# Optimization experiments

Hardware: AMD Instinct MI355X
Metric: run time of the kernel (lower is better)

The kernel has to match this reference:

```python
import jax, jax.numpy as jnp
import numpy as np
import math

B, H, N, D = 8, 8, 4096, 64
M = 64          # select_number (CUR rank)
N_ITER = 6      # Newton-Schulz iterations in iterative_inv


def setup_inputs() -> dict:
    key = jax.random.key(0)
    k1, k2, k3 = jax.random.split(key, 3)
    Q = jax.random.normal(k1, (B, H, N, D), jnp.float32)
    K = jax.random.normal(k2, (B, H, N, D), jnp.float32)
    V = jax.random.normal(k3, (B, H, N, D), jnp.float32)
    mask = jnp.ones((B, N), dtype=bool)
    return {"Q": Q, "K": K, "V": V, "mask": mask}


def _top_k_sum_select(T, mask, m):
    # select_type='sum', absolute=False -> score = row sum over D
    somme = T.sum(-1)                                    # [B,H,N]
    somme = jnp.where(mask[:, None, :], somme, -jnp.finfo(somme.dtype).max)
    idx = jnp.argsort(-somme, axis=-1)[..., :m]          # descending top-m, [B,H,M]
    nt = jnp.take_along_axis(T, idx[..., None], axis=2)  # [B,H,M,D]
    return nt, idx


def _iterative_inv(mat, n_iter=N_ITER):
    # init_option='original': global-max scaled transpose
    m = mat.shape[-1]
    I = jnp.eye(m, dtype=mat.dtype)
    Km = mat
    Vm = Km.swapaxes(-1, -2) / jnp.max(Km.sum(-2))
    for _ in range(n_iter):
        KV = Km @ Vm
        Vm = 0.25 * Vm @ (13.0 * I - KV @ (15.0 * I - KV @ (7.0 * I - KV)))
    return Vm


def reference(Q, K, V, mask):
    Qs = Q / math.sqrt(D)
    nc, _ = _top_k_sum_select(K, mask, M)        # column landmarks of K
    nr, r_idx = _top_k_sum_select(Qs, mask, M)   # row landmarks of Q
    c = jnp.einsum('bhnd,bhmd->bhnm', Qs, nc)    # [B,H,N,M]
    r = jnp.einsum('bhmd,bhnd->bhmn', nr, K)     # [B,H,M,N]
    r = jnp.where(mask[:, None, None, :], r, -jnp.finfo(r.dtype).max)
    kernel_1 = jax.nn.softmax(c, axis=-1)        # [B,H,N,M]
    # m_matrix_composition: gather rows of kernel_1 at r_idx -> [B,H,M,M]
    u = jnp.take_along_axis(kernel_1, r_idx[..., None], axis=2)
    kernel_3 = jax.nn.softmax(r, axis=-1)        # [B,H,M,N]
    kernel_2_inv = _iterative_inv(u)             # [B,H,M,M]
    RV = kernel_3 @ V                            # [B,H,M,D]
    X = kernel_1 @ (kernel_2_inv @ RV)           # [B,H,N,D]
    return X
```

## Files before the change

kernel.cpp:

```cpp
#include <hip/hip_runtime.h>
#include <math.h>

#define NSEQ 4096

#define OFF_SUMK 0u
#define OFF_SUMQ 262144u
#define OFF_WTH  0u
#define OFF_WTL  131072u
#define OFF_U    262144u
#define OFF_NC   524288u
#define OFF_NR   786432u
#define OFF_VM   1048576u
#define OFF_NCH  1310720u
#define OFF_NCL  1441792u
#define OFF_PMAX 1572864u
#define OFF_PSUM 1638400u
#define OFF_HMAX 1703936u
#define OFF_PRV  1704000u

typedef unsigned short u16;
typedef short short8 __attribute__((ext_vector_type(8)));
typedef short bf4 __attribute__((ext_vector_type(4)));
typedef float f32x4 __attribute__((ext_vector_type(4)));

__device__ __forceinline__ u16 f2bf(float x) {
    unsigned u = __float_as_uint(x);
    unsigned r = (u + 0x7FFFu + ((u >> 16) & 1u)) >> 16;
    return (u16)r;
}
__device__ __forceinline__ void splitbf(float x, u16& h, u16& l) {
    unsigned u = __float_as_uint(x);
    h = (u16)(u >> 16);
    float hf = __uint_as_float(u & 0xFFFF0000u);
    l = f2bf(x - hf);
}

__device__ __forceinline__ short8 ldfrag(const u16* base, int row, int k0) {
    int byte = (row << 7) + (k0 << 1);
    byte ^= (row & 7) << 4;
    return *(const short8*)((const char*)base + byte);
}
__device__ __forceinline__ void st4(u16* base, int row, int c0, ushort4 v) {
    int byte = (row << 7) + (c0 << 1);
    byte ^= (row & 7) << 4;
    *(ushort4*)((char*)base + byte) = v;
}
__device__ __forceinline__ void stb16(u16* base, int row, int c, u16 v) {
    int byte = (row << 7) + (c << 1);
    byte ^= (row & 7) << 4;
    *(u16*)((char*)base + byte) = v;
}
__device__ __forceinline__ unsigned vt_byte(int d, int n) {
    unsigned byte = ((unsigned)d << 7) + ((unsigned)n << 1);
    byte ^= ((d & 7) << 4) | ((d & 8) << 3);
    return byte;
}

__device__ __forceinline__ f32x4 MFMA(short8 a, short8 b, f32x4 c) {
    return __builtin_amdgcn_mfma_f32_16x16x32_bf16(a, b, c, 0, 0, 0);
}

__device__ __forceinline__ void stage64(const float* __restrict__ g, u16* Lh, u16* Ll,
                                        int t, float scale) {
#pragma unroll
    for (int i = 0; i < 4; i++) {
        int e = t + 256 * i;
        int row = e >> 4, c0 = (e & 15) << 2;
        float4 v = *(const float4*)(g + row * 64 + c0);
        float vv[4] = {v.x * scale, v.y * scale, v.z * scale, v.w * scale};
        ushort4 h, l;
        splitbf(vv[0], h.x, l.x); splitbf(vv[1], h.y, l.y);
        splitbf(vv[2], h.z, l.z); splitbf(vv[3], h.w, l.w);
        st4(Lh, row, c0, h); st4(Ll, row, c0, l);
    }
}

__device__ __forceinline__ void copy64bf(u16* dst, const u16* __restrict__ src, int t) {
#pragma unroll
    for (int i = 0; i < 4; i++) {
        int e = t + 256 * i;
        int row = e >> 4, c0 = (e & 15) << 2;
        ushort4 v = *(const ushort4*)(src + row * 64 + c0);
        st4(dst, row, c0, v);
    }
}

__device__ __forceinline__ void loadT64(float* dst, const float* __restrict__ src, int t) {
    for (int e = t; e < 1024; e += 256) {
        int m = e >> 4, k0 = (e & 15) << 2;
        float4 v = *(const float4*)(src + m * 64 + k0);
        dst[(k0 + 0) * 64 + m] = v.x;
        dst[(k0 + 1) * 64 + m] = v.y;
        dst[(k0 + 2) * 64 + m] = v.z;
        dst[(k0 + 3) * 64 + m] = v.w;
    }
}
__device__ __forceinline__ void mm64add(const float* Acm, const float* Brm,
                                        float acc[4][4], int i0, int j0) {
#pragma unroll 8
    for (int k = 0; k < 64; k++) {
        float4 a = *(const float4*)(Acm + k * 64 + i0);
        float4 b = *(const float4*)(Brm + k * 64 + j0);
        acc[0][0] += a.x * b.x; acc[0][1] += a.x * b.y; acc[0][2] += a.x * b.z; acc[0][3] += a.x * b.w;
        acc[1][0] += a.y * b.x; acc[1][1] += a.y * b.y; acc[1][2] += a.y * b.z; acc[1][3] += a.y * b.w;
        acc[2][0] += a.z * b.x; acc[2][1] += a.z * b.y; acc[2][2] += a.z * b.z; acc[2][3] += a.z * b.w;
        acc[3][0] += a.w * b.x; acc[3][1] += a.w * b.y; acc[3][2] += a.w * b.z; acc[3][3] += a.w * b.w;
    }
}
__device__ __forceinline__ void mm64(const float* Acm, const float* Brm,
                                     float acc[4][4], int i0, int j0) {
#pragma unroll
    for (int r = 0; r < 4; r++)
#pragma unroll
        for (int c = 0; c < 4; c++) acc[r][c] = 0.f;
    mm64add(Acm, Brm, acc, i0, j0);
}
__device__ __forceinline__ void writeN64(float* dst, const float acc[4][4], int i0, int j0, float s) {
#pragma unroll
    for (int r = 0; r < 4; r++) {
        float4 v;
        v.x = s * acc[r][0]; v.y = s * acc[r][1]; v.z = s * acc[r][2]; v.w = s * acc[r][3];
        *(float4*)(dst + (i0 + r) * 64 + j0) = v;
    }
}

__global__ __launch_bounds__(256) void k_sums(const float* __restrict__ Qg,
                                              const float* __restrict__ Kg, float* ws) {
    size_t row = (size_t)blockIdx.x * 64 + (threadIdx.x >> 2);
    int q = threadIdx.x & 3;
    const float4* qp = (const float4*)(Qg + row * 64 + q * 16);
    const float4* kp = (const float4*)(Kg + row * 64 + q * 16);
    float s1 = 0.f, s2 = 0.f;
#pragma unroll
    for (int i = 0; i < 4; i++) { float4 v = qp[i]; s1 += (v.x + v.y) + (v.z + v.w); }
#pragma unroll
    for (int i = 0; i < 4; i++) { float4 v = kp[i]; s2 += (v.x + v.y) + (v.z + v.w); }
    s1 += __shfl_xor(s1, 1); s1 += __shfl_xor(s1, 2);
    s2 += __shfl_xor(s2, 1); s2 += __shfl_xor(s2, 2);
    if (q == 0) { ws[OFF_SUMQ + row] = s1; ws[OFF_SUMK + row] = s2; }
}

__global__ __launch_bounds__(256) void k_select(const float* __restrict__ Qg,
                                                const float* __restrict__ Kg, float* ws) {
    int head = blockIdx.x, sel = blockIdx.y, t = threadIdx.x;
    __shared__ int hist[257];
    __shared__ int idx_s[64];
    __shared__ unsigned s_prefix;
    __shared__ int s_need, s_cnt, s_win;
    __shared__ int wred[4];
    const float* scores = ws + (sel ? OFF_SUMQ : OFF_SUMK) + (size_t)head * 4096;
    unsigned uu[16];
#pragma unroll
    for (int i = 0; i < 16; i++) {
        unsigned u = __float_as_uint(scores[t + 256 * i]);
        uu[i] = (u & 0x80000000u) ? ~u : (u | 0x80000000u);
    }
    if (t == 0) { s_prefix = 0u; s_need = 64; }
    __syncthreads();
#pragma unroll
    for (int p = 0; p < 4; p++) {
        hist[t] = 0;
        if (t == 0) hist[256] = 0;
        __syncthreads();
        unsigned pref = s_prefix;
        int sh = 32 - 8 * p;
        int dsh = 24 - 8 * p;
#pragma unroll
        for (int i = 0; i < 16; i++) {
            bool active = (p == 0) || ((uu[i] >> sh) == (pref >> sh));
            if (active) atomicAdd(&hist[(uu[i] >> dsh) & 255], 1);
        }
        __syncthreads();
        for (int s = 1; s < 256; s <<= 1) {
            int v = (t + s < 256) ? hist[t + s] : 0;
            __syncthreads();
            hist[t] += v;
            __syncthreads();
        }
        int need = s_need;
        __syncthreads();
        if (hist[t] >= need && (t == 255 || hist[t + 1] < need)) {
            s_need = need - ((t == 255) ? 0 : hist[t + 1]);
            s_prefix = pref | ((unsigned)t << dsh);
        }
        __syncthreads();
    }
    unsigned thr = s_prefix;
    int needEq = s_need;
    if (t == 0) s_cnt = 0;
    __syncthreads();
    unsigned eqm = 0;
#pragma unroll
    for (int i = 0; i < 16; i++) {
        if (uu[i] > thr) { int pos = atomicAdd(&s_cnt, 1); idx_s[pos] = t + 256 * i; }
        else if (uu[i] == thr) eqm |= (1u << i);
    }
    __syncthreads();
    int base = 64 - needEq;
    int lane = t & 63, wid = t >> 6;
    for (int r = 0; r < needEq; r++) {
        int mymin = 0x7FFFFFFF;
#pragma unroll
        for (int i = 0; i < 16; i++)
            if ((eqm >> i) & 1) mymin = min(mymin, t + 256 * i);
#pragma unroll
        for (int s = 1; s < 64; s <<= 1) mymin = min(mymin, __shfl_xor(mymin, s));
        if (lane == 0) wred[wid] = mymin;
        __syncthreads();
        if (t == 0) {
            int wv = min(min(wred[0], wred[1]), min(wred[2], wred[3]));
            s_win = wv;
            idx_s[base + r] = wv;
        }
        __syncthreads();
        int wv = s_win;
        if ((wv & 255) == t) eqm &= ~(1u << (wv >> 8));
        __syncthreads();
    }
    const float* src = sel ? Qg : Kg;
    float* dst = ws + (sel ? OFF_NR : OFF_NC) + (size_t)head * 4096;
    u16* dh = (u16*)(ws + OFF_NCH) + (size_t)head * 4096;
    u16* dl = (u16*)(ws + OFF_NCL) + (size_t)head * 4096;
    float scl = sel ? 0.125f : 1.0f;
    for (int e = t; e < 4096; e += 256) {
        int m = e >> 6, d = e & 63;
        float v = src[((size_t)head * NSEQ + (size_t)idx_s[m]) * 64 + d] * scl;
        dst[e] = v;
        if (!sel) { u16 h, l; splitbf(v, h, l); dh[e] = h; dl[e] = l; }
    }
}

__global__ __launch_bounds__(256) void k_u(float* ws) {
    int head = blockIdx.x, t = threadIdx.x;
    __shared__ __align__(16) float A_s[4096];
    __shared__ __align__(16) float B_s[4096];
    __shared__ float colpart[1024];
    loadT64(A_s, ws + OFF_NR + (size_t)head * 4096, t);
    loadT64(B_s, ws + OFF_NC + (size_t)head * 4096, t);
    __syncthreads();
    int ti = t >> 4, tj = t & 15, i0 = ti << 2, j0 = tj << 2;
    float acc[4][4];
    mm64(A_s, B_s, acc, i0, j0);
#pragma unroll
    for (int r = 0; r < 4; r++) {
        float m0 = fmaxf(fmaxf(acc[r][0], acc[r][1]), fmaxf(acc[r][2], acc[r][3]));
        m0 = fmaxf(m0, __shfl_xor(m0, 1)); m0 = fmaxf(m0, __shfl_xor(m0, 2));
        m0 = fmaxf(m0, __shfl_xor(m0, 4)); m0 = fmaxf(m0, __shfl_xor(m0, 8));
        float s = 0.f;
#pragma unroll
        for (int c = 0; c < 4; c++) { acc[r][c] = __expf(acc[r][c] - m0); s += acc[r][c]; }
        s += __shfl_xor(s, 1); s += __shfl_xor(s, 2);
        s += __shfl_xor(s, 4); s += __shfl_xor(s, 8);
#pragma unroll
        for (int c = 0; c < 4; c++) acc[r][c] = acc[r][c] / s;
    }
    float* u = ws + OFF_U + (size_t)head * 4096;
#pragma unroll
    for (int r = 0; r < 4; r++) {
        float4 v; v.x = acc[r][0]; v.y = acc[r][1]; v.z = acc[r][2]; v.w = acc[r][3];
        *(float4*)(u + (i0 + r) * 64 + j0) = v;
    }
#pragma unroll
    for (int c = 0; c < 4; c++)
        colpart[ti * 64 + j0 + c] = acc[0][c] + acc[1][c] + acc[2][c] + acc[3][c];
    __syncthreads();
    if (t < 64) {
        float cs = 0.f;
#pragma unroll
        for (int g = 0; g < 16; g++) cs += colpart[g * 64 + t];
        float v = cs;
#pragma unroll
        for (int s = 1; s < 64; s <<= 1) v = fmaxf(v, __shfl_xor(v, s));
        if (t == 0) ws[OFF_HMAX + head] = v;
    }
}

__global__ __launch_bounds__(256) void k_nsinv(float* ws) {
    int head = blockIdx.x, t = threadIdx.x;
    __shared__ __align__(16) u16 KmH[4096], KmL[4096];
    __shared__ __align__(16) u16 VmNH[4096], VmNL[4096];
    __shared__ __align__(16) u16 VmTH[4096], VmTL[4096];
    __shared__ __align__(16) u16 KVH[4096], KVL[4096];
    __shared__ __align__(16) u16 BtH[4096], BtL[4096];
    __shared__ __align__(16) float Vmf[4096];

    int w = t >> 6, lane = t & 63, lrow = lane & 15, lk = (lane >> 4) << 3;
    int mrow0 = 16 * w + ((lane >> 4) << 2);

    float g = ws[OFF_HMAX + lane];
#pragma unroll
    for (int s = 1; s < 64; s <<= 1) g = fmaxf(g, __shfl_xor(g, s));
    float ginv = 1.0f / g;

    const float* u = ws + OFF_U + (size_t)head * 4096;
#pragma unroll
    for (int i = 0; i < 4; i++) {
        int e = t + 256 * i;
        int row = e >> 4, c0 = (e & 15) << 2;
        float4 v = *(const float4*)(u + row * 64 + c0);
        float vv[4] = {v.x, v.y, v.z, v.w};
        ushort4 h4, l4;
        splitbf(vv[0], h4.x, l4.x); splitbf(vv[1], h4.y, l4.y);
        splitbf(vv[2], h4.z, l4.z); splitbf(vv[3], h4.w, l4.w);
        st4(KmH, row, c0, h4); st4(KmL, row, c0, l4);
        float sv[4] = {vv[0] * ginv, vv[1] * ginv, vv[2] * ginv, vv[3] * ginv};
        splitbf(sv[0], h4.x, l4.x); splitbf(sv[1], h4.y, l4.y);
        splitbf(sv[2], h4.z, l4.z); splitbf(sv[3], h4.w, l4.w);
        st4(VmTH, row, c0, h4); st4(VmTL, row, c0, l4);
#pragma unroll
        for (int k = 0; k < 4; k++) {
            u16 h, l; splitbf(sv[k], h, l);
            stb16(VmNH, c0 + k, row, h); stb16(VmNL, c0 + k, row, l);
            Vmf[(c0 + k) * 64 + row] = sv[k];
        }
    }
    __syncthreads();

    f32x4 cv[4];
    for (int it = 0; it < 6; it++) {
        {
            short8 a0h = ldfrag(KmH, 16 * w + lrow, lk);
            short8 a0l = ldfrag(KmL, 16 * w + lrow, lk);
            short8 a1h = ldfrag(KmH, 16 * w + lrow, 32 + lk);
            short8 a1l = ldfrag(KmL, 16 * w + lrow, 32 + lk);
#pragma unroll
            for (int nt = 0; nt < 4; nt++) {
                f32x4 acc = (f32x4){0.f, 0.f, 0.f, 0.f};
                short8 bh = ldfrag(VmTH, 16 * nt + lrow, lk);
                short8 bl = ldfrag(VmTL, 16 * nt + lrow, lk);
                acc = MFMA(a0h, bh, acc); acc = MFMA(a0l, bh, acc); acc = MFMA(a0h, bl, acc);
                bh = ldfrag(VmTH, 16 * nt + lrow, 32 + lk);
                bl = ldfrag(VmTL, 16 * nt + lrow, 32 + lk);
                acc = MFMA(a1h, bh, acc); acc = MFMA(a1l, bh, acc); acc = MFMA(a1h, bl, acc);
                cv[nt] = acc;
            }
        }
#pragma unroll
        for (int nt = 0; nt < 4; nt++)
#pragma unroll
            for (int j = 0; j < 4; j++) {
                int m = mrow0 + j, n = 16 * nt + lrow;
                float v = cv[nt][j];
                u16 h, l; splitbf(v, h, l);
                stb16(KVH, m, n, h); stb16(KVL, m, n, l);
                float b = ((m == n) ? 7.f : 0.f) - v;
                splitbf(b, h, l);
                stb16(BtH, n, m, h); stb16(BtL, n, m, l);
            }
        __syncthreads();
        {
            short8 a0h = ldfrag(KVH, 16 * w + lrow, lk);
            short8 a0l = ldfrag(KVL, 16 * w + lrow, lk);
            short8 a1h = ldfrag(KVH, 16 * w + lrow, 32 + lk);
            short8 a1l = ldfrag(KVL, 16 * w + lrow, 32 + lk);
#pragma unroll
            for (int nt = 0; nt < 4; nt++) {
                f32x4 acc = (f32x4){0.f, 0.f, 0.f, 0.f};
                short8 bh = ldfrag(BtH, 16 * nt + lrow, lk);
                short8 bl = ldfrag(BtL, 16 * nt + lrow, lk);
                acc = MFMA(a0h, bh, acc); acc = MFMA(a0l, bh, acc); acc = MFMA(a0h, bl, acc);
                bh = ldfrag(BtH, 16 * nt + lrow, 32 + lk);
                bl = ldfrag(BtL, 16 * nt + lrow, 32 + lk);
                acc = MFMA(a1h, bh, acc); acc = MFMA(a1l, bh, acc); acc = MFMA(a1h, bl, acc);
                cv[nt] = acc;
            }
        }
        __syncthreads();
#pragma unroll
        for (int nt = 0; nt < 4; nt++)
#pragma unroll
            for (int j = 0; j < 4; j++) {
                int m = mrow0 + j, n = 16 * nt + lrow;
                float b = ((m == n) ? 15.f : 0.f) - cv[nt][j];
                u16 h, l; splitbf(b, h, l);
                stb16(BtH, n, m, h); stb16(BtL, n, m, l);
            }
        __syncthreads();
        {
            short8 a0h = ldfrag(KVH, 16 * w + lrow, lk);
            short8 a0l = ldfrag(KVL, 16 * w + lrow, lk);
            short8 a1h = ldfrag(KVH, 16 * w + lrow, 32 + lk);
            short8 a1l = ldfrag(KVL, 16 * w + lrow, 32 + lk);
#pragma unroll
            for (int nt = 0; nt < 4; nt++) {
                f32x4 acc = (f32x4){0.f, 0.f, 0.f, 0.f};
                short8 bh = ldfrag(BtH, 16 * nt + lrow, lk);
                short8 bl = ldfrag(BtL, 16 * nt + lrow, lk);
                acc = MFMA(a0h, bh, acc); acc = MFMA(a0l, bh, acc); acc = MFMA(a0h, bl, acc);
                bh = ldfrag(BtH, 16 * nt + lrow, 32 + lk);
                bl = ldfrag(BtL, 16 * nt + lrow, 32 + lk);
                acc = MFMA(a1h, bh, acc); acc = MFMA(a1l, bh, acc); acc = MFMA(a1h, bl, acc);
                cv[nt] = acc;
            }
        }
        __syncthreads();
#pragma unroll
        for (int nt = 0; nt < 4; nt++)
#pragma unroll
            for (int j = 0; j < 4; j++) {
                int m = mrow0 + j, n = 16 * nt + lrow;
                float b = ((m == n) ? 13.f : 0.f) - cv[nt][j];
                u16 h, l; splitbf(b, h, l);
                stb16(BtH, n, m, h); stb16(BtL, n, m, l);
            }
        __syncthreads();
        {
            short8 a0h = ldfrag(VmNH, 16 * w + lrow, lk);
            short8 a0l = ldfrag(VmNL, 16 * w + lrow, lk);
            short8 a1h = ldfrag(VmNH, 16 * w + lrow, 32 + lk);
            short8 a1l = ldfrag(VmNL, 16 * w + lrow, 32 + lk);
#pragma unroll
            for (int nt = 0; nt < 4; nt++) {
                f32x4 acc = (f32x4){0.f, 0.f, 0.f, 0.f};
                short8 bh = ldfrag(BtH, 16 * nt + lrow, lk);
                short8 bl = ldfrag(BtL, 16 * nt + lrow, lk);
                acc = MFMA(a0h, bh, acc); acc = MFMA(a0l, bh, acc); acc = MFMA(a0h, bl, acc);
                bh = ldfrag(BtH, 16 * nt + lrow, 32 + lk);
                bl = ldfrag(BtL, 16 * nt + lrow, 32 + lk);
                acc = MFMA(a1h, bh, acc); acc = MFMA(a1l, bh, acc); acc = MFMA(a1h, bl, acc);
                cv[nt] = acc;
            }
        }
        __syncthreads();
#pragma unroll
        for (int nt = 0; nt < 4; nt++)
#pragma unroll
            for (int j = 0; j < 4; j++) {
                int m = mrow0 + j, n = 16 * nt + lrow;
                float v = 0.25f * cv[nt][j];
                u16 h, l; splitbf(v, h, l);
                stb16(VmNH, m, n, h); stb16(VmNL, m, n, l);
                stb16(VmTH, n, m, h); stb16(VmTL, n, m, l);
                Vmf[m * 64 + n] = v;
            }
        __syncthreads();
    }

    float* vm = ws + OFF_VM + (size_t)head * 4096;
#pragma unroll
    for (int i = 0; i < 4; i++) {
        int e = t + 256 * i;
        int row = e >> 4, c0 = (e & 15) << 2;
        *(float4*)(vm + row * 64 + c0) = *(const float4*)(Vmf + row * 64 + c0);
    }
}

__global__ __launch_bounds__(256) void k_rvp(const float* __restrict__ Kg,
                                             const float* __restrict__ Vg, float* ws) {
    int head = blockIdx.x, ch = blockIdx.y, t = threadIdx.x;
    int nch = gridDim.y;
    int nsub = (NSEQ / 64) / nch;
    __shared__ __align__(16) u16 Kh[4096], Kl[4096];
    __shared__ __align__(16) u16 Vth[4096], Vtl[4096];
    int w = t >> 6, lane = t & 63, lrow = lane & 15, g = lane >> 4;
    int lk = g << 3;
    int mrow0 = 16 * w + (g << 2);

    short8 nh0, nl0, nh1, nl1;
    {
        const float* nr = ws + OFF_NR + (size_t)head * 4096 + (size_t)(16 * w + lrow) * 64;
        float a[8], b[8];
        *(float4*)(a + 0) = *(const float4*)(nr + lk);
        *(float4*)(a + 4) = *(const float4*)(nr + lk + 4);
        *(float4*)(b + 0) = *(const float4*)(nr + 32 + lk);
        *(float4*)(b + 4) = *(const float4*)(nr + 32 + lk + 4);
#pragma unroll
        for (int i = 0; i < 8; i++) {
            u16 h, l;
            splitbf(a[i], h, l); nh0[i] = (short)h; nl0[i] = (short)l;
            splitbf(b[i], h, l); nh1[i] = (short)h; nl1[i] = (short)l;
        }
    }

    f32x4 rv[4];
#pragma unroll
    for (int dt = 0; dt < 4; dt++) rv[dt] = (f32x4){0.f, 0.f, 0.f, 0.f};
    float mrow = -INFINITY, srow = 0.f;

    int rows = NSEQ / nch;
    const float* Kb = Kg + ((size_t)head * NSEQ + (size_t)ch * rows) * 64;
    const float* Vb = Vg + ((size_t)head * NSEQ + (size_t)ch * rows) * 64;
    int vd = lane;
    int nb4 = (t >> 6) << 2;

    for (int s8 = 0; s8 < nsub; s8++) {
        __syncthreads();
        stage64(Kb + s8 * 4096, Kh, Kl, t, 1.0f);
        const float* Vs = Vb + s8 * 4096;
#pragma unroll
        for (int i = 0; i < 4; i++) {
            int n0 = nb4 + 16 * i;
            float x0 = Vs[(n0 + 0) * 64 + vd];
            float x1 = Vs[(n0 + 1) * 64 + vd];
            float x2 = Vs[(n0 + 2) * 64 + vd];
            float x3 = Vs[(n0 + 3) * 64 + vd];
            ushort4 h4, l4;
            splitbf(x0, h4.x, l4.x); splitbf(x1, h4.y, l4.y);
            splitbf(x2, h4.z, l4.z); splitbf(x3, h4.w, l4.w);
            *(ushort4*)((char*)Vth + vt_byte(vd, n0)) = h4;
            *(ushort4*)((char*)Vtl + vt_byte(vd, n0)) = l4;
        }
        __syncthreads();

        f32x4 cv[4];
#pragma unroll
        for (int nt = 0; nt < 4; nt++) {
            f32x4 acc = (f32x4){0.f, 0.f, 0.f, 0.f};
            short8 ah = ldfrag(Kh, 16 * nt + lrow, lk);
            short8 al = ldfrag(Kl, 16 * nt + lrow, lk);
            acc = MFMA(ah, nh0, acc); acc = MFMA(al, nh0, acc); acc = MFMA(ah, nl0, acc);
            ah = ldfrag(Kh, 16 * nt + lrow, 32 + lk);
            al = ldfrag(Kl, 16 * nt + lrow, 32 + lk);
            acc = MFMA(ah, nh1, acc); acc = MFMA(al, nh1, acc); acc = MFMA(ah, nl1, acc);
            cv[nt] = acc;
        }
        float m0 = cv[0][0];
#pragma unroll
        for (int nt = 0; nt < 4; nt++)
#pragma unroll
            for (int j = 0; j < 4; j++) m0 = fmaxf(m0, cv[nt][j]);
        m0 = fmaxf(m0, __shfl_xor(m0, 16));
        m0 = fmaxf(m0, __shfl_xor(m0, 32));
        float mnew = fmaxf(mrow, m0);
        float sc = __expf(mrow - mnew);
        float ps = 0.f;
#pragma unroll
        for (int nt = 0; nt < 4; nt++)
#pragma unroll
            for (int j = 0; j < 4; j++) {
                float p = __expf(cv[nt][j] - mnew);
                cv[nt][j] = p; ps += p;
            }
        ps += __shfl_xor(ps, 16);
        ps += __shfl_xor(ps, 32);
        srow = srow * sc + ps;
        mrow = mnew;
        float scl[4];
#pragma unroll
        for (int j = 0; j < 4; j++) scl[j] = __shfl(sc, (g << 2) + j);
#pragma unroll
        for (int dt = 0; dt < 4; dt++)
#pragma unroll
            for (int j = 0; j < 4; j++) rv[dt][j] *= scl[j];
        short8 pah[2], pal[2];
#pragma unroll
        for (int h2 = 0; h2 < 2; h2++)
#pragma unroll
            for (int i = 0; i < 8; i++) {
                u16 hh, ll;
                splitbf(cv[2 * h2 + (i >> 2)][i & 3], hh, ll);
                pah[h2][i] = (short)hh; pal[h2][i] = (short)ll;
            }
#pragma unroll
        for (int dt = 0; dt < 4; dt++) {
            int drow = 16 * dt + lrow;
#pragma unroll
            for (int h2 = 0; h2 < 2; h2++) {
                bf4 xh0 = *(const bf4*)((const char*)Vth + vt_byte(drow, 32 * h2 + 4 * g));
                bf4 xh1 = *(const bf4*)((const char*)Vth + vt_byte(drow, 32 * h2 + 16 + 4 * g));
                bf4 xl0 = *(const bf4*)((const char*)Vtl + vt_byte(drow, 32 * h2 + 4 * g));
                bf4 xl1 = *(const bf4*)((const char*)Vtl + vt_byte(drow, 32 * h2 + 16 + 4 * g));
                short8 bh = __builtin_shufflevector(xh0, xh1, 0, 1, 2, 3, 4, 5, 6, 7);
                short8 bl = __builtin_shufflevector(xl0, xl1, 0, 1, 2, 3, 4, 5, 6, 7);
                rv[dt] = MFMA(pah[h2], bh, rv[dt]);
                rv[dt] = MFMA(pal[h2], bh, rv[dt]);
                rv[dt] = MFMA(pah[h2], bl, rv[dt]);
            }
        }
    }
    size_t pb = (size_t)(head * nch + ch) * 64;
    if (lane < 16) {
        ws[OFF_PMAX + pb + 16 * w + lane] = mrow;
        ws[OFF_PSUM + pb + 16 * w + lane] = srow;
    }
#pragma unroll
    for (int dt = 0; dt < 4; dt++)
#pragma unroll
        for (int j = 0; j < 4; j++)
            ws[OFF_PRV + (pb + mrow0 + j) * 64 + 16 * dt + lrow] = rv[dt][j];
}

__global__ __launch_bounds__(256) void k_comb(float* ws, int nch) {
    int head = blockIdx.x, t = threadIdx.x;
    __shared__ __align__(16) float A_s[4096];
    __shared__ __align__(16) float B_s[4096];
    loadT64(A_s, ws + OFF_VM + (size_t)head * 4096, t);
    int ti = t >> 4, tj = t & 15, i0 = ti << 2, j0 = tj << 2;
    const float* pm = ws + OFF_PMAX + (size_t)head * nch * 64;
    const float* psv = ws + OFF_PSUM + (size_t)head * nch * 64;
    const float* prv = ws + OFF_PRV + (size_t)head * nch * 4096;
    float gm[4] = {-INFINITY, -INFINITY, -INFINITY, -INFINITY};
    for (int c8 = 0; c8 < nch; c8++)
#pragma unroll
        for (int r = 0; r < 4; r++) gm[r] = fmaxf(gm[r], pm[c8 * 64 + i0 + r]);
    float stot[4] = {0.f, 0.f, 0.f, 0.f};
    float racc[4][4];
#pragma unroll
    for (int r = 0; r < 4; r++)
#pragma unroll
        for (int c = 0; c < 4; c++) racc[r][c] = 0.f;
    for (int c8 = 0; c8 < nch; c8++) {
#pragma unroll
        for (int r = 0; r < 4; r++) {
            float w = __expf(pm[c8 * 64 + i0 + r] - gm[r]);
            stot[r] += w * psv[c8 * 64 + i0 + r];
            float4 v = *(const float4*)(prv + (size_t)(c8 * 64 + i0 + r) * 64 + j0);
            racc[r][0] += w * v.x; racc[r][1] += w * v.y;
            racc[r][2] += w * v.z; racc[r][3] += w * v.w;
        }
    }
#pragma unroll
    for (int r = 0; r < 4; r++)
#pragma unroll
        for (int c = 0; c < 4; c++) racc[r][c] /= stot[r];
    writeN64(B_s, racc, i0, j0, 1.f);
    __syncthreads();
    float acc[4][4];
    mm64(A_s, B_s, acc, i0, j0);
    u16* wth = (u16*)(ws + OFF_WTH) + (size_t)head * 4096;
    u16* wtl = (u16*)(ws + OFF_WTL) + (size_t)head * 4096;
#pragma unroll
    for (int r = 0; r < 4; r++)
#pragma unroll
        for (int c = 0; c < 4; c++) {
            u16 h, l; splitbf(acc[r][c], h, l);
            wth[(j0 + c) * 64 + (i0 + r)] = h;
            wtl[(j0 + c) * 64 + (i0 + r)] = l;
        }
}

__global__ __launch_bounds__(256) void k_final(const float* __restrict__ Qg, float* ws,
                                               float* __restrict__ out) {
    int tile = blockIdx.x, head = blockIdx.y, t = threadIdx.x;
    __shared__ __align__(16) u16 Ah[4096], Al[4096];
    __shared__ __align__(16) u16 Bh[4096], Bl[4096];
    __shared__ __align__(16) float C[64 * 68];
    const float* Qt = Qg + ((size_t)head * NSEQ + (size_t)tile * 64) * 64;
    stage64(Qt, Ah, Al, t, 0.125f);
    copy64bf(Bh, (const u16*)(ws + OFF_NCH) + (size_t)head * 4096, t);
    copy64bf(Bl, (const u16*)(ws + OFF_NCL) + (size_t)head * 4096, t);
    __syncthreads();
    int w = t >> 6, lane = t & 63, lrow = lane & 15, lk = (lane >> 4) << 3;
    int mrow0 = 16 * w + ((lane >> 4) << 2);
    short8 a0h = ldfrag(Ah, 16 * w + lrow, lk);
    short8 a0l = ldfrag(Al, 16 * w + lrow, lk);
    short8 a1h = ldfrag(Ah, 16 * w + lrow, 32 + lk);
    short8 a1l = ldfrag(Al, 16 * w + lrow, 32 + lk);
    f32x4 sa[4];
#pragma unroll
    for (int nt = 0; nt < 4; nt++) {
        f32x4 acc = (f32x4){0.f, 0.f, 0.f, 0.f};
        short8 bh = ldfrag(Bh, 16 * nt + lrow, lk);
        short8 bl = ldfrag(Bl, 16 * nt + lrow, lk);
        acc = MFMA(a0h, bh, acc); acc = MFMA(a0l, bh, acc); acc = MFMA(a0h, bl, acc);
        bh = ldfrag(Bh, 16 * nt + lrow, 32 + lk);
        bl = ldfrag(Bl, 16 * nt + lrow, 32 + lk);
        acc = MFMA(a1h, bh, acc); acc = MFMA(a1l, bh, acc); acc = MFMA(a1h, bl, acc);
        sa[nt] = acc;
    }
#pragma unroll
    for (int j = 0; j < 4; j++) {
        float m0 = fmaxf(fmaxf(sa[0][j], sa[1][j]), fmaxf(sa[2][j], sa[3][j]));
        m0 = fmaxf(m0, __shfl_xor(m0, 1)); m0 = fmaxf(m0, __shfl_xor(m0, 2));
        m0 = fmaxf(m0, __shfl_xor(m0, 4)); m0 = fmaxf(m0, __shfl_xor(m0, 8));
        float ps = 0.f;
#pragma unroll
        for (int nt = 0; nt < 4; nt++) {
            float p = __expf(sa[nt][j] - m0);
            sa[nt][j] = p; ps += p;
        }
        ps += __shfl_xor(ps, 1); ps += __shfl_xor(ps, 2);
        ps += __shfl_xor(ps, 4); ps += __shfl_xor(ps, 8);
        float inv = 1.f / ps;
#pragma unroll
        for (int nt = 0; nt < 4; nt++) sa[nt][j] *= inv;
    }
    __syncthreads();
#pragma unroll
    for (int nt = 0; nt < 4; nt++)
#pragma unroll
        for (int j = 0; j < 4; j++) {
            u16 h, l; splitbf(sa[nt][j], h, l);
            stb16(Ah, mrow0 + j, 16 * nt + lrow, h);
            stb16(Al, mrow0 + j, 16 * nt + lrow, l);
        }
    copy64bf(Bh, (const u16*)(ws + OFF_WTH) + (size_t)head * 4096, t);
    copy64bf(Bl, (const u16*)(ws + OFF_WTL) + (size_t)head * 4096, t);
    __syncthreads();
    short8 p0h = ldfrag(Ah, 16 * w + lrow, lk);
    short8 p0l = ldfrag(Al, 16 * w + lrow, lk);
    short8 p1h = ldfrag(Ah, 16 * w + lrow, 32 + lk);
    short8 p1l = ldfrag(Al, 16 * w + lrow, 32 + lk);
#pragma unroll
    for (int dt = 0; dt < 4; dt++) {
        f32x4 x = (f32x4){0.f, 0.f, 0.f, 0.f};
        short8 bh = ldfrag(Bh, 16 * dt + lrow, lk);
        short8 bl = ldfrag(Bl, 16 * dt + lrow, lk);
        x = MFMA(p0h, bh, x); x = MFMA(p0l, bh, x); x = MFMA(p0h, bl, x);
        bh = ldfrag(Bh, 16 * dt + lrow, 32 + lk);
        bl = ldfrag(Bl, 16 * dt + lrow, 32 + lk);
        x = MFMA(p1h, bh, x); x = MFMA(p1l, bh, x); x = MFMA(p1h, bl, x);
#pragma unroll
        for (int j = 0; j < 4; j++) C[(mrow0 + j) * 68 + 16 * dt + lrow] = x[j];
    }
    __syncthreads();
    float* op = out + ((size_t)head * NSEQ + (size_t)tile * 64) * 64;
#pragma unroll
    for (int i = 0; i < 4; i++) {
        int e = t + 256 * i;
        int row = e >> 4, c0 = (e & 15) << 2;
        *(float4*)(op + row * 64 + c0) = *(const float4*)(C + row * 68 + c0);
    }
}

extern "C" void kernel_launch(void* const* d_in, const int* in_sizes, int n_in,
                              void* d_out, int out_size, void* d_ws, size_t ws_size,
                              hipStream_t stream) {
    const float* Q = (const float*)d_in[0];
    const float* K = (const float*)d_in[1];
    const float* V = (const float*)d_in[2];
    float* ws = (float*)d_ws;
    float* out = (float*)d_out;

    size_t need16 = ((size_t)OFF_PRV + 64ull * 16ull * 4096ull) * sizeof(float);
    int nch = (ws_size >= need16) ? 16 : 8;

    k_sums<<<4096, 256, 0, stream>>>(Q, K, ws);
    k_select<<<dim3(64, 2), 256, 0, stream>>>(Q, K, ws);
    k_u<<<64, 256, 0, stream>>>(ws);
    k_rvp<<<dim3(64, nch), 256, 0, stream>>>(K, V, ws);
    k_nsinv<<<64, 256, 0, stream>>>(ws);
    k_comb<<<64, 256, 0, stream>>>(ws, nch);
    k_final<<<dim3(64, 64), 256, 0, stream>>>(Q, ws, out);
}
```

Before: 180.0 us.

## Register-prefetch next K/V tile in k_rvp and fix chunk count at 8

k_rvp now loads the next 64-row K and V tiles into registers with vectorized float4 reads while the MFMA work on the current tile runs, so global load latency is hidden behind compute. V is now read as float4 per thread and transposed in registers instead of with scalar strided loads, and the V transpose swizzle is changed to match the new store pattern. The chunk count is fixed at compile time to 8 instead of choosing 16 when the workspace allows it. This halves k_rvp's grid, which may reduce parallelism, and adds register pressure from the prefetch buffers.

```diff
diff --git a/kernel.cpp b/kernel.cpp
--- a/kernel.cpp
+++ b/kernel.cpp
@@ -2,6 +2,7 @@
 #include <math.h>
 
 #define NSEQ 4096
+#define NCH  8
 
 #define OFF_SUMK 0u
 #define OFF_SUMQ 262144u
@@ -52,7 +53,7 @@
 }
 __device__ __forceinline__ unsigned vt_byte(int d, int n) {
     unsigned byte = ((unsigned)d << 7) + ((unsigned)n << 1);
-    byte ^= ((d & 7) << 4) | ((d & 8) << 3);
+    byte ^= (unsigned)(d & 15) << 3;
     return byte;
 }
 
@@ -448,13 +449,14 @@
 __global__ __launch_bounds__(256) void k_rvp(const float* __restrict__ Kg,
                                              const float* __restrict__ Vg, float* ws) {
     int head = blockIdx.x, ch = blockIdx.y, t = threadIdx.x;
-    int nch = gridDim.y;
-    int nsub = (NSEQ / 64) / nch;
+    const int nsub = (NSEQ / 64) / NCH;
     __shared__ __align__(16) u16 Kh[4096], Kl[4096];
     __shared__ __align__(16) u16 Vth[4096], Vtl[4096];
     int w = t >> 6, lane = t & 63, lrow = lane & 15, g = lane >> 4;
     int lk = g << 3;
     int mrow0 = 16 * w + (g << 2);
+    int krow = t >> 4, kc0 = (t & 15) << 2;
+    int vn0 = (t & 15) << 2, vd0 = (t >> 4) << 2;
 
     short8 nh0, nl0, nh1, nl1;
     {
@@ -477,30 +479,50 @@
     for (int dt = 0; dt < 4; dt++) rv[dt] = (f32x4){0.f, 0.f, 0.f, 0.f};
     float mrow = -INFINITY, srow = 0.f;
 
-    int rows = NSEQ / nch;
+    const int rows = NSEQ / NCH;
     const float* Kb = Kg + ((size_t)head * NSEQ + (size_t)ch * rows) * 64;
     const float* Vb = Vg + ((size_t)head * NSEQ + (size_t)ch * rows) * 64;
-    int vd = lane;
-    int nb4 = (t >> 6) << 2;
+
+    float4 kreg[4], vreg[4];
+#pragma unroll
+    for (int i = 0; i < 4; i++)
+        kreg[i] = *(const float4*)(Kb + (krow + 16 * i) * 64 + kc0);
+#pragma unroll
+    for (int k = 0; k < 4; k++)
+        vreg[k] = *(const float4*)(Vb + (vn0 + k) * 64 + vd0);
 
     for (int s8 = 0; s8 < nsub; s8++) {
-        __syncthreads();
-        stage64(Kb + s8 * 4096, Kh, Kl, t, 1.0f);
-        const float* Vs = Vb + s8 * 4096;
 #pragma unroll
         for (int i = 0; i < 4; i++) {
-            int n0 = nb4 + 16 * i;
-            float x0 = Vs[(n0 + 0) * 64 + vd];
-            float x1 = Vs[(n0 + 1) * 64 + vd];
-            float x2 = Vs[(n0 + 2) * 64 + vd];
-            float x3 = Vs[(n0 + 3) * 64 + vd];
+            ushort4 h4, l4;
+            splitbf(kreg[i].x, h4.x, l4.x); splitbf(kreg[i].y, h4.y, l4.y);
+            splitbf(kreg[i].z, h4.z, l4.z); splitbf(kreg[i].w, h4.w, l4.w);
+            st4(Kh, krow + 16 * i, kc0, h4); st4(Kl, krow + 16 * i, kc0, l4);
+        }
+#pragma unroll
+        for (int dd = 0; dd < 4; dd++) {
+            float x0 = ((const float*)&vreg[0])[dd];
+            float x1 = ((const float*)&vreg[1])[dd];
+            float x2 = ((const float*)&vreg[2])[dd];
+            float x3 = ((const float*)&vreg[3])[dd];
             ushort4 h4, l4;
             splitbf(x0, h4.x, l4.x); splitbf(x1, h4.y, l4.y);
             splitbf(x2, h4.z, l4.z); splitbf(x3, h4.w, l4.w);
-            *(ushort4*)((char*)Vth + vt_byte(vd, n0)) = h4;
-            *(ushort4*)((char*)Vtl + vt_byte(vd, n0)) = l4;
-        }
-        __syncthreads();
+            unsigned byte = vt_byte(vd0 + dd, vn0);
+            *(ushort4*)((char*)Vth + byte) = h4;
+            *(ushort4*)((char*)Vtl + byte) = l4;
+        }
+        __syncthreads();
+        if (s8 + 1 < nsub) {
+            const float* Kn = Kb + (s8 + 1) * 4096;
+            const float* Vn = Vb + (s8 + 1) * 4096;
+#pragma unroll
+            for (int i = 0; i < 4; i++)
+                kreg[i] = *(const float4*)(Kn + (krow + 16 * i) * 64 + kc0);
+#pragma unroll
+            for (int k = 0; k < 4; k++)
+                vreg[k] = *(const float4*)(Vn + (vn0 + k) * 64 + vd0);
+        }
 
         f32x4 cv[4];
 #pragma unroll
@@ -567,8 +589,9 @@
                 rv[dt] = MFMA(pah[h2], bl, rv[dt]);
             }
         }
-    }
-    size_t pb = (size_t)(head * nch + ch) * 64;
+        __syncthreads();
+    }
+    size_t pb = (size_t)(head * NCH + ch) * 64;
     if (lane < 16) {
         ws[OFF_PMAX + pb + 16 * w + lane] = mrow;
         ws[OFF_PSUM + pb + 16 * w + lane] = srow;
@@ -580,8 +603,9 @@
             ws[OFF_PRV + (pb + mrow0 + j) * 64 + 16 * dt + lrow] = rv[dt][j];
 }
 
-__global__ __launch_bounds__(256) void k_comb(float* ws, int nch) {
+__global__ __launch_bounds__(256) void k_comb(float* ws) {
     int head = blockIdx.x, t = threadIdx.x;
+    const int nch = NCH;
     __shared__ __align__(16) float A_s[4096];
     __shared__ __align__(16) float B_s[4096];
     loadT64(A_s, ws + OFF_VM + (size_t)head * 4096, t);
@@ -722,14 +746,11 @@
     float* ws = (float*)d_ws;
     float* out = (float*)d_out;
 
-    size_t need16 = ((size_t)OFF_PRV + 64ull * 16ull * 4096ull) * sizeof(float);
-    int nch = (ws_size >= need16) ? 16 : 8;
-
     k_sums<<<4096, 256, 0, stream>>>(Q, K, ws);
     k_select<<<dim3(64, 2), 256, 0, stream>>>(Q, K, ws);
     k_u<<<64, 256, 0, stream>>>(ws);
-    k_rvp<<<dim3(64, nch), 256, 0, stream>>>(K, V, ws);
+    k_rvp<<<dim3(64, NCH), 256, 0, stream>>>(K, V, ws);
     k_nsinv<<<64, 256, 0, stream>>>(ws);
-    k_comb<<<64, 256, 0, stream>>>(ws, nch);
+    k_comb<<<64, 256, 0, stream>>>(ws);
     k_final<<<dim3(64, 64), 256, 0, stream>>>(Q, ws, out);
 }
```

Result: faster. 144.7 us (-19.6%).
